# Optimization experiments

Hardware: AMD Instinct MI355X
Metric: run time of the kernel (lower is better)

## Reference

```python
import jax, jax.numpy as jnp
import numpy as np

N, E = 50000, 800000
IN, MID, OUT = 128, 256, 128
LN_EPS = 1e-5


def layer_norm(x, gamma, beta, eps=LN_EPS):
    mu = jnp.mean(x, axis=-1, keepdims=True)
    var = jnp.mean(jnp.square(x - mu), axis=-1, keepdims=True)
    return (x - mu) * jax.lax.rsqrt(var + eps) * gamma + beta


def gcn_conv(x, W, b, src, dst, norm, n):
    # x' = D^{-1/2}(A+I)D^{-1/2} X W + b  (self-loops already folded into src/dst/norm)
    h = x @ W                                  # [N, F_out]
    msg = h[src] * norm[:, None]               # [E+N, F_out] gather + scale
    out = jax.ops.segment_sum(msg, dst, num_segments=n)
    return out + b


def setup_inputs() -> dict:
    key = jax.random.key(0)
    ks = jax.random.split(key, 4)
    x = jax.random.normal(ks[0], (N, IN), dtype=jnp.float32)
    edge_index = jax.random.randint(ks[1], (2, E), 0, N, dtype=jnp.int32)
    W1 = jax.random.normal(ks[2], (IN, MID), dtype=jnp.float32) * (1.0 / np.sqrt(IN))
    b1 = jnp.zeros((MID,), jnp.float32)
    g1 = jnp.ones((IN,), jnp.float32)
    be1 = jnp.zeros((IN,), jnp.float32)
    W4 = jax.random.normal(ks[3], (MID, OUT), dtype=jnp.float32) * (1.0 / np.sqrt(MID))
    b4 = jnp.zeros((OUT,), jnp.float32)
    g4 = jnp.ones((MID,), jnp.float32)
    be4 = jnp.zeros((MID,), jnp.float32)
    return {"x": x, "W1": W1, "b1": b1, "g1": g1, "be1": be1,
            "W4": W4, "b4": b4, "g4": g4, "be4": be4,
            "edge_index": edge_index}


def reference(x, W1, b1, g1, be1, W4, b4, g4, be4, edge_index):
    n = x.shape[0]
    loop = jnp.arange(n, dtype=edge_index.dtype)
    src = jnp.concatenate([edge_index[0], loop])   # [E+N]
    dst = jnp.concatenate([edge_index[1], loop])   # [E+N]
    deg = jax.ops.segment_sum(jnp.ones_like(src, x.dtype), dst, num_segments=n)
    dinv = jax.lax.rsqrt(deg)                      # deg >= 1 thanks to self-loops
    norm = dinv[src] * dinv[dst]                   # [E+N]

    h = gcn_conv(layer_norm(x, g1, be1), W1, b1, src, dst, norm, n)
    h = jax.nn.gelu(h, approximate=False)          # torch F.gelu default = exact erf
    h = gcn_conv(layer_norm(h, g4, be4), W4, b4, src, dst, norm, n)
    return h
```

## Files before the change

### kernel.cpp

```cpp
#include <hip/hip_runtime.h>
#include <math.h>

#define N_NODES 50000
#define E_EDGES 800000

typedef __attribute__((ext_vector_type(4))) float f32x4;
typedef __attribute__((ext_vector_type(8))) short s16x8;

#define T1_OFF    0UL
#define AGG1_OFF  12800000UL
#define T2B_OFF   38400000UL
#define WB1H_OFF  64000000UL
#define WB1L_OFF  64100096UL
#define WB4H_OFF  64200192UL
#define WB4L_OFF  64300288UL
#define DINV_OFF  64400384UL
#define HIST8_OFF 64600384UL
#define RP8_OFF   66200384UL
#define POSREL_OFF 67800448UL
#define CSRS_OFF  71000448UL
#define BSUM_OFF  74200448UL

__device__ __forceinline__ float lo16f(unsigned u) { return __uint_as_float(u << 16); }
__device__ __forceinline__ float hi16f(unsigned u) { return __uint_as_float(u & 0xffff0000u); }
__device__ __forceinline__ unsigned pack2bf(float a, float b) {
  unsigned ua = __float_as_uint(a); ua += 0x7fffu + ((ua >> 16) & 1u);
  unsigned ub = __float_as_uint(b); ub += 0x7fffu + ((ub >> 16) & 1u);
  return (ua >> 16) | (ub & 0xffff0000u);
}
__device__ __forceinline__ float gelu_f(float x) {
  return 0.5f * x * (1.f + erff(x * 0.70710678118654752f));
}

__global__ __launch_bounds__(256) void zero_hist8(int4* __restrict__ h) {
  int i = blockIdx.x * 256 + threadIdx.x;
  if (i < 100000) h[i] = make_int4(0, 0, 0, 0);
}

__global__ __launch_bounds__(256) void edge_pos(const int* __restrict__ dst,
                                                int* __restrict__ hist8,
                                                int* __restrict__ posrel) {
  int e = blockIdx.x * 256 + threadIdx.x;
  int d = dst[e];
  int seg = blockIdx.x & 7;
  int r = atomicAdd(&hist8[d * 8 + seg], 1);
  __builtin_nontemporal_store(r, posrel + e);
}

__global__ __launch_bounds__(1024) void scan_partial(const int* __restrict__ hist,
                                                     int* __restrict__ rp,
                                                     int* __restrict__ bsum, int n) {
  __shared__ int wsum[16];
  int tid = threadIdx.x, lane = tid & 63, wv = tid >> 6;
  int i = blockIdx.x * 1024 + tid;
  int v = (i < n) ? hist[i] : 0;
  int sc = v;
  #pragma unroll
  for (int m = 1; m < 64; m <<= 1) { int o = __shfl_up(sc, m); if (lane >= m) sc += o; }
  if (lane == 63) wsum[wv] = sc;
  __syncthreads();
  if (wv == 0) {
    int w = (lane < 16) ? wsum[lane] : 0;
    int swc = w;
    #pragma unroll
    for (int m = 1; m < 16; m <<= 1) { int o = __shfl_up(swc, m); if (lane >= m) swc += o; }
    if (lane < 16) wsum[lane] = swc - w;
    if (lane == 15) bsum[blockIdx.x] = swc;
  }
  __syncthreads();
  if (i < n) rp[i] = (sc - v) + wsum[wv];
}

__global__ __launch_bounds__(64) void scan_bsums(int* __restrict__ bsum, int nb) {
  int lane = threadIdx.x;
  int carry = 0;
  for (int base = 0; base < nb; base += 64) {
    int i = base + lane;
    int v = (i < nb) ? bsum[i] : 0;
    int sc = v;
    #pragma unroll
    for (int m = 1; m < 64; m <<= 1) { int o = __shfl_up(sc, m); if (lane >= m) sc += o; }
    if (i < nb) bsum[i] = carry + sc - v;
    carry += __shfl(sc, 63);
  }
  if (lane == 0) bsum[nb] = carry;
}

__global__ __launch_bounds__(1024) void scan_add(int* __restrict__ rp,
                                                 const int* __restrict__ bsum, int n) {
  int i = blockIdx.x * 1024 + threadIdx.x;
  if (i < n) rp[i] += bsum[blockIdx.x];
  if (i == 0) rp[n] = bsum[gridDim.x];
}

__global__ __launch_bounds__(256) void dinv_kernel(const int* __restrict__ rp8,
                                                   float* __restrict__ dinv, int n) {
  int i = blockIdx.x * 256 + threadIdx.x;
  if (i < n) {
    int deg = rp8[i * 8 + 8] - rp8[i * 8];
    dinv[i] = rsqrtf((float)(deg + 1));
  }
}

__global__ __launch_bounds__(256) void fill2(const int* __restrict__ src,
                                             const int* __restrict__ dst,
                                             const int* __restrict__ rp8,
                                             const int* __restrict__ posrel,
                                             int* __restrict__ csr_src) {
  int e = blockIdx.x * 256 + threadIdx.x;
  int s = src[e], d = dst[e];
  int seg = blockIdx.x & 7;
  int pos = rp8[d * 8 + seg] + posrel[e];
  __builtin_nontemporal_store(s, csr_src + pos);
}

__global__ __launch_bounds__(256) void convW_split(const float* __restrict__ W,
                                                   unsigned* __restrict__ Wh,
                                                   unsigned* __restrict__ Wl, int K, int N) {
  int tid = blockIdx.x * 256 + threadIdx.x;
  if (tid >= (K * N) / 8) return;
  int c15 = tid & 15;
  int kg  = (tid >> 4) & 3;
  int KS  = K >> 5;
  int ks  = (tid >> 6) % KS;
  int nt  = (tid >> 6) / KS;
  int col = nt * 16 + c15;
  int k0  = ks * 32 + kg * 8;
  float w[8];
  #pragma unroll
  for (int j = 0; j < 8; ++j) w[j] = W[(size_t)(k0 + j) * N + col];
  uint4 h, l;
  h.x = pack2bf(w[0], w[1]); l.x = pack2bf(w[0] - lo16f(h.x), w[1] - hi16f(h.x));
  h.y = pack2bf(w[2], w[3]); l.y = pack2bf(w[2] - lo16f(h.y), w[3] - hi16f(h.y));
  h.z = pack2bf(w[4], w[5]); l.z = pack2bf(w[4] - lo16f(h.z), w[5] - hi16f(h.z));
  h.w = pack2bf(w[6], w[7]); l.w = pack2bf(w[6] - lo16f(h.w), w[7] - hi16f(h.w));
  *reinterpret_cast<uint4*>(Wh + (size_t)tid * 4) = h;
  *reinterpret_cast<uint4*>(Wl + (size_t)tid * 4) = l;
}

__global__ __launch_bounds__(256) void ln1_kernel(const float* __restrict__ x,
                                                  const float* __restrict__ g,
                                                  const float* __restrict__ be,
                                                  unsigned* __restrict__ T) {
  int lane = threadIdx.x & 63, wv = threadIdx.x >> 6;
  int row = blockIdx.x * 4 + wv;
  float2 v = *reinterpret_cast<const float2*>(x + (size_t)row * 128 + lane * 2);
  float s = v.x + v.y, sq = v.x * v.x + v.y * v.y;
  #pragma unroll
  for (int m = 1; m < 64; m <<= 1) { s += __shfl_xor(s, m); sq += __shfl_xor(sq, m); }
  float mu = s * (1.f / 128.f);
  float var = sq * (1.f / 128.f) - mu * mu;
  float rs = rsqrtf(var + 1e-5f);
  float2 gg = *reinterpret_cast<const float2*>(g + lane * 2);
  float2 bb = *reinterpret_cast<const float2*>(be + lane * 2);
  T[(size_t)row * 64 + lane] =
      pack2bf((v.x - mu) * rs * gg.x + bb.x, (v.y - mu) * rs * gg.y + bb.y);
}

template <int MODE>
__global__ __launch_bounds__(256) void agg128(const unsigned* __restrict__ T,
                                              const int* __restrict__ rp8,
                                              const int* __restrict__ csr_src,
                                              const float* __restrict__ dinv,
                                              const float* __restrict__ b,
                                              float* __restrict__ out) {
  int lane = threadIdx.x & 63, wv = threadIdx.x >> 6;
  int node = blockIdx.x * 4 + wv;
  float di = dinv[node], sn = di * di;
  unsigned us = T[(size_t)node * 64 + lane];
  float a0 = lo16f(us) * sn, a1 = hi16f(us) * sn;
  int e = rp8[node * 8], e1 = rp8[node * 8 + 8];
  for (; e + 3 < e1; e += 4) {
    int4 c = *reinterpret_cast<const int4*>(csr_src + e);
    unsigned u0 = T[(size_t)c.x * 64 + lane];
    unsigned u1 = T[(size_t)c.y * 64 + lane];
    unsigned u2 = T[(size_t)c.z * 64 + lane];
    unsigned u3 = T[(size_t)c.w * 64 + lane];
    float n0 = dinv[c.x] * di, n1 = dinv[c.y] * di;
    float n2 = dinv[c.z] * di, n3 = dinv[c.w] * di;
    a0 += lo16f(u0) * n0; a1 += hi16f(u0) * n0;
    a0 += lo16f(u1) * n1; a1 += hi16f(u1) * n1;
    a0 += lo16f(u2) * n2; a1 += hi16f(u2) * n2;
    a0 += lo16f(u3) * n3; a1 += hi16f(u3) * n3;
  }
  for (; e < e1; ++e) {
    int s = csr_src[e];
    unsigned u = T[(size_t)s * 64 + lane];
    float nr = dinv[s] * di;
    a0 += lo16f(u) * nr; a1 += hi16f(u) * nr;
  }
  if (MODE == 0) {
    *reinterpret_cast<float2*>(out + (size_t)node * 128 + lane * 2) = make_float2(a0, a1);
  } else {
    float2 bb = *reinterpret_cast<const float2*>(b + lane * 2);
    *reinterpret_cast<float2*>(out + (size_t)node * 128 + lane * 2) =
        make_float2(a0 + bb.x, a1 + bb.y);
  }
}

__global__ __launch_bounds__(256) void gemm1_fused(const float* __restrict__ A,
                                                   const unsigned* __restrict__ Wh,
                                                   const unsigned* __restrict__ Wl,
                                                   const float* __restrict__ b,
                                                   const float* __restrict__ g,
                                                   const float* __restrict__ be,
                                                   unsigned* __restrict__ T2b, int n) {
  __shared__ float st[32 * 260];
  int t = threadIdx.x, lane = t & 63, w = t >> 6;
  int rtile = (w >> 1) * 16;
  int c0 = (w & 1) * 128;
  int arow = blockIdx.x * 32 + rtile + (lane & 15);
  if (arow >= n) arow = n - 1;
  const float* aptr = A + (size_t)arow * 128 + (lane >> 4) * 8;
  f32x4 acc[8];
  #pragma unroll
  for (int nf = 0; nf < 8; ++nf) acc[nf] = (f32x4)(0.f);
  #pragma unroll
  for (int ks = 0; ks < 4; ++ks) {
    float4 v0 = *reinterpret_cast<const float4*>(aptr + ks * 32);
    float4 v1 = *reinterpret_cast<const float4*>(aptr + ks * 32 + 4);
    uint4 h, l;
    h.x = pack2bf(v0.x, v0.y); l.x = pack2bf(v0.x - lo16f(h.x), v0.y - hi16f(h.x));
    h.y = pack2bf(v0.z, v0.w); l.y = pack2bf(v0.z - lo16f(h.y), v0.w - hi16f(h.y));
    h.z = pack2bf(v1.x, v1.y); l.z = pack2bf(v1.x - lo16f(h.z), v1.y - hi16f(h.z));
    h.w = pack2bf(v1.z, v1.w); l.w = pack2bf(v1.z - lo16f(h.w), v1.w - hi16f(h.w));
    s16x8 ah = *reinterpret_cast<s16x8*>(&h);
    s16x8 al = *reinterpret_cast<s16x8*>(&l);
    #pragma unroll
    for (int nf = 0; nf < 8; ++nf) {
      int nt = (c0 >> 4) + nf;
      size_t bo = (size_t)(((nt * 4 + ks) * 4 + (lane >> 4)) * 16 + (lane & 15)) * 4;
      s16x8 bh = *reinterpret_cast<const s16x8*>(Wh + bo);
      s16x8 bl = *reinterpret_cast<const s16x8*>(Wl + bo);
      acc[nf] = __builtin_amdgcn_mfma_f32_16x16x32_bf16(ah, bh, acc[nf], 0, 0, 0);
      acc[nf] = __builtin_amdgcn_mfma_f32_16x16x32_bf16(al, bh, acc[nf], 0, 0, 0);
      acc[nf] = __builtin_amdgcn_mfma_f32_16x16x32_bf16(ah, bl, acc[nf], 0, 0, 0);
    }
  }
  #pragma unroll
  for (int nf = 0; nf < 8; ++nf) {
    int col = c0 + nf * 16 + (lane & 15);
    float bb = b[col];
    #pragma unroll
    for (int r = 0; r < 4; ++r) {
      int row = rtile + (lane >> 4) * 4 + r;
      st[row * 260 + col] = gelu_f(acc[nf][r] + bb);
    }
  }
  __syncthreads();
  float4 gg = *reinterpret_cast<const float4*>(g + lane * 4);
  float4 bb2 = *reinterpret_cast<const float4*>(be + lane * 4);
  #pragma unroll
  for (int rr = 0; rr < 8; ++rr) {
    int row = w * 8 + rr;
    float4 v = *reinterpret_cast<const float4*>(&st[row * 260 + lane * 4]);
    float s = v.x + v.y + v.z + v.w;
    float sq = v.x * v.x + v.y * v.y + v.z * v.z + v.w * v.w;
    #pragma unroll
    for (int m = 1; m < 64; m <<= 1) { s += __shfl_xor(s, m); sq += __shfl_xor(sq, m); }
    float mu = s * (1.f / 256.f);
    float var = sq * (1.f / 256.f) - mu * mu;
    float rs = rsqrtf(var + 1e-5f);
    int gr = blockIdx.x * 32 + row;
    if (gr < n) {
      uint2 p;
      p.x = pack2bf((v.x - mu) * rs * gg.x + bb2.x, (v.y - mu) * rs * gg.y + bb2.y);
      p.y = pack2bf((v.z - mu) * rs * gg.z + bb2.z, (v.w - mu) * rs * gg.w + bb2.w);
      *reinterpret_cast<uint2*>(T2b + (size_t)gr * 128 + lane * 2) = p;
    }
  }
}

__global__ __launch_bounds__(256) void gemm2_mfma(const unsigned* __restrict__ Ab,
                                                  const unsigned* __restrict__ Wh,
                                                  const unsigned* __restrict__ Wl,
                                                  unsigned* __restrict__ T2, int n) {
  __shared__ float st[32 * 132];
  int t = threadIdx.x, lane = t & 63, w = t >> 6;
  int rtile = (w >> 1) * 16;
  int c0 = (w & 1) * 64;
  int arow = blockIdx.x * 32 + rtile + (lane & 15);
  if (arow >= n) arow = n - 1;
  const unsigned* aptr = Ab + (size_t)arow * 128 + (lane >> 4) * 4;
  f32x4 acc[4];
  #pragma unroll
  for (int nf = 0; nf < 4; ++nf) acc[nf] = (f32x4)(0.f);
  #pragma unroll
  for (int ks = 0; ks < 8; ++ks) {
    s16x8 af = *reinterpret_cast<const s16x8*>(aptr + ks * 16);
    #pragma unroll
    for (int nf = 0; nf < 4; ++nf) {
      int nt = (c0 >> 4) + nf;
      size_t bo = (size_t)(((nt * 8 + ks) * 4 + (lane >> 4)) * 16 + (lane & 15)) * 4;
      s16x8 bh = *reinterpret_cast<const s16x8*>(Wh + bo);
      s16x8 bl = *reinterpret_cast<const s16x8*>(Wl + bo);
      acc[nf] = __builtin_amdgcn_mfma_f32_16x16x32_bf16(af, bh, acc[nf], 0, 0, 0);
      acc[nf] = __builtin_amdgcn_mfma_f32_16x16x32_bf16(af, bl, acc[nf], 0, 0, 0);
    }
  }
  #pragma unroll
  for (int nf = 0; nf < 4; ++nf) {
    int col = c0 + nf * 16 + (lane & 15);
    #pragma unroll
    for (int r = 0; r < 4; ++r) {
      int row = rtile + (lane >> 4) * 4 + r;
      st[row * 132 + col] = acc[nf][r];
    }
  }
  __syncthreads();
  #pragma unroll
  for (int rr = 0; rr < 8; ++rr) {
    int row = w * 8 + rr;
    int gr = blockIdx.x * 32 + row;
    if (gr < n) {
      float2 v = *reinterpret_cast<const float2*>(&st[row * 132 + lane * 2]);
      T2[(size_t)gr * 64 + lane] = pack2bf(v.x, v.y);
    }
  }
}

extern "C" void kernel_launch(void* const* d_in, const int* in_sizes, int n_in,
                              void* d_out, int out_size, void* d_ws, size_t ws_size,
                              hipStream_t stream) {
  (void)in_sizes; (void)n_in; (void)out_size; (void)ws_size;
  const float* x   = (const float*)d_in[0];
  const float* W1  = (const float*)d_in[1];
  const float* b1  = (const float*)d_in[2];
  const float* g1  = (const float*)d_in[3];
  const float* be1 = (const float*)d_in[4];
  const float* W4  = (const float*)d_in[5];
  const float* b4  = (const float*)d_in[6];
  const float* g4  = (const float*)d_in[7];
  const float* be4 = (const float*)d_in[8];
  const int*   ei  = (const int*)d_in[9];
  const int* src = ei;
  const int* dst = ei + E_EDGES;

  char* ws = (char*)d_ws;
  unsigned* T1    = (unsigned*)(ws + T1_OFF);
  unsigned* T2    = (unsigned*)(ws + T1_OFF);
  float*    AGG1  = (float*)(ws + AGG1_OFF);
  unsigned* T2b   = (unsigned*)(ws + T2B_OFF);
  unsigned* Wb1h  = (unsigned*)(ws + WB1H_OFF);
  unsigned* Wb1l  = (unsigned*)(ws + WB1L_OFF);
  unsigned* Wb4h  = (unsigned*)(ws + WB4H_OFF);
  unsigned* Wb4l  = (unsigned*)(ws + WB4L_OFF);
  float* dinv     = (float*)(ws + DINV_OFF);
  int*   hist8    = (int*)(ws + HIST8_OFF);
  int*   rp8      = (int*)(ws + RP8_OFF);
  int*   posrel   = (int*)(ws + POSREL_OFF);
  int*   csr_src  = (int*)(ws + CSRS_OFF);
  int*   bsum     = (int*)(ws + BSUM_OFF);
  float* outp     = (float*)d_out;

  const int NSEG = N_NODES * 8;
  int nblkE  = E_EDGES / 256;
  int nbScan = (NSEG + 1023) / 1024;
  int nblkG  = (N_NODES + 31) / 32;

  hipLaunchKernelGGL(zero_hist8, dim3(391), dim3(256), 0, stream, (int4*)hist8);
  hipLaunchKernelGGL(edge_pos, dim3(nblkE), dim3(256), 0, stream, dst, hist8, posrel);
  hipLaunchKernelGGL(scan_partial, dim3(nbScan), dim3(1024), 0, stream, hist8, rp8, bsum, NSEG);
  hipLaunchKernelGGL(scan_bsums, dim3(1), dim3(64), 0, stream, bsum, nbScan);
  hipLaunchKernelGGL(scan_add, dim3(nbScan), dim3(1024), 0, stream, rp8, bsum, NSEG);
  hipLaunchKernelGGL(dinv_kernel, dim3((N_NODES + 255) / 256), dim3(256), 0, stream,
                     rp8, dinv, N_NODES);
  hipLaunchKernelGGL(fill2, dim3(nblkE), dim3(256), 0, stream, src, dst, rp8, posrel, csr_src);
  hipLaunchKernelGGL(convW_split, dim3(16), dim3(256), 0, stream, W1, Wb1h, Wb1l, 128, 256);
  hipLaunchKernelGGL(convW_split, dim3(16), dim3(256), 0, stream, W4, Wb4h, Wb4l, 256, 128);

  hipLaunchKernelGGL(ln1_kernel, dim3(N_NODES / 4), dim3(256), 0, stream, x, g1, be1, T1);
  hipLaunchKernelGGL(agg128<0>, dim3(N_NODES / 4), dim3(256), 0, stream,
                     T1, rp8, csr_src, dinv, (const float*)nullptr, AGG1);
  hipLaunchKernelGGL(gemm1_fused, dim3(nblkG), dim3(256), 0, stream,
                     AGG1, Wb1h, Wb1l, b1, g4, be4, T2b, N_NODES);

  hipLaunchKernelGGL(gemm2_mfma, dim3(nblkG), dim3(256), 0, stream, T2b, Wb4h, Wb4l, T2, N_NODES);
  hipLaunchKernelGGL(agg128<2>, dim3(N_NODES / 4), dim3(256), 0, stream,
                     T2, rp8, csr_src, dinv, b4, outp);
}
```

Baseline: 234.0 us.

## Emit split-bf16 aggregates and retile GEMM warps to reuse weight fragments

The first aggregation now writes its fp32 result as pre-split bf16 hi/lo arrays, so gemm1 no longer converts fp32 A on the fly. Both GEMMs are retiled so each warp covers 32 rows and a narrower column band, which halves the per-warp weight-fragment loads relative to the MFMA count. The degree computation now reads the per-node histogram directly instead of the scanned row pointers. Storage for the intermediate stays the same size, but gemm1's A is now read from two arrays and the split rounding happens in the aggregation epilogue.

```diff
diff --git a/kernel.cpp b/kernel.cpp
--- a/kernel.cpp
+++ b/kernel.cpp
@@ -8,7 +8,8 @@
 typedef __attribute__((ext_vector_type(8))) short s16x8;
 
 #define T1_OFF    0UL
-#define AGG1_OFF  12800000UL
+#define A1H_OFF   12800000UL
+#define A1L_OFF   25600000UL
 #define T2B_OFF   38400000UL
 #define WB1H_OFF  64000000UL
 #define WB1L_OFF  64100096UL
@@ -93,11 +94,13 @@
   if (i == 0) rp[n] = bsum[gridDim.x];
 }
 
-__global__ __launch_bounds__(256) void dinv_kernel(const int* __restrict__ rp8,
+__global__ __launch_bounds__(256) void dinv_kernel(const int* __restrict__ hist8,
                                                    float* __restrict__ dinv, int n) {
   int i = blockIdx.x * 256 + threadIdx.x;
   if (i < n) {
-    int deg = rp8[i * 8 + 8] - rp8[i * 8];
+    int4 a = *reinterpret_cast<const int4*>(hist8 + i * 8);
+    int4 b = *reinterpret_cast<const int4*>(hist8 + i * 8 + 4);
+    int deg = a.x + a.y + a.z + a.w + b.x + b.y + b.z + b.w;
     dinv[i] = rsqrtf((float)(deg + 1));
   }
 }
@@ -163,7 +166,9 @@
                                               const int* __restrict__ csr_src,
                                               const float* __restrict__ dinv,
                                               const float* __restrict__ b,
-                                              float* __restrict__ out) {
+                                              float* __restrict__ out,
+                                              unsigned* __restrict__ outh,
+                                              unsigned* __restrict__ outl) {
   int lane = threadIdx.x & 63, wv = threadIdx.x >> 6;
   int node = blockIdx.x * 4 + wv;
   float di = dinv[node], sn = di * di;
@@ -190,7 +195,10 @@
     a0 += lo16f(u) * nr; a1 += hi16f(u) * nr;
   }
   if (MODE == 0) {
-    *reinterpret_cast<float2*>(out + (size_t)node * 128 + lane * 2) = make_float2(a0, a1);
+    unsigned h = pack2bf(a0, a1);
+    float r0 = a0 - lo16f(h), r1 = a1 - hi16f(h);
+    outh[(size_t)node * 64 + lane] = h;
+    outl[(size_t)node * 64 + lane] = pack2bf(r0, r1);
   } else {
     float2 bb = *reinterpret_cast<const float2*>(b + lane * 2);
     *reinterpret_cast<float2*>(out + (size_t)node * 128 + lane * 2) =
@@ -198,7 +206,8 @@
   }
 }
 
-__global__ __launch_bounds__(256) void gemm1_fused(const float* __restrict__ A,
+__global__ __launch_bounds__(256) void gemm1_fused(const unsigned* __restrict__ Ah,
+                                                   const unsigned* __restrict__ Al,
                                                    const unsigned* __restrict__ Wh,
                                                    const unsigned* __restrict__ Wl,
                                                    const float* __restrict__ b,
@@ -207,46 +216,56 @@
                                                    unsigned* __restrict__ T2b, int n) {
   __shared__ float st[32 * 260];
   int t = threadIdx.x, lane = t & 63, w = t >> 6;
-  int rtile = (w >> 1) * 16;
-  int c0 = (w & 1) * 128;
-  int arow = blockIdx.x * 32 + rtile + (lane & 15);
-  if (arow >= n) arow = n - 1;
-  const float* aptr = A + (size_t)arow * 128 + (lane >> 4) * 8;
-  f32x4 acc[8];
-  #pragma unroll
-  for (int nf = 0; nf < 8; ++nf) acc[nf] = (f32x4)(0.f);
+  int kg = lane >> 4, c15 = lane & 15;
+  int c0 = w * 64;
+  int row0 = blockIdx.x * 32 + c15;
+  int r0 = min(row0, n - 1);
+  int r1 = min(row0 + 16, n - 1);
+  const unsigned* ah0 = Ah + (size_t)r0 * 64 + kg * 4;
+  const unsigned* al0 = Al + (size_t)r0 * 64 + kg * 4;
+  const unsigned* ah1 = Ah + (size_t)r1 * 64 + kg * 4;
+  const unsigned* al1 = Al + (size_t)r1 * 64 + kg * 4;
+  f32x4 acc[2][4];
+  #pragma unroll
+  for (int rt = 0; rt < 2; ++rt)
+    #pragma unroll
+    for (int nf = 0; nf < 4; ++nf) acc[rt][nf] = (f32x4)(0.f);
   #pragma unroll
   for (int ks = 0; ks < 4; ++ks) {
-    float4 v0 = *reinterpret_cast<const float4*>(aptr + ks * 32);
-    float4 v1 = *reinterpret_cast<const float4*>(aptr + ks * 32 + 4);
-    uint4 h, l;
-    h.x = pack2bf(v0.x, v0.y); l.x = pack2bf(v0.x - lo16f(h.x), v0.y - hi16f(h.x));
-    h.y = pack2bf(v0.z, v0.w); l.y = pack2bf(v0.z - lo16f(h.y), v0.w - hi16f(h.y));
-    h.z = pack2bf(v1.x, v1.y); l.z = pack2bf(v1.x - lo16f(h.z), v1.y - hi16f(h.z));
-    h.w = pack2bf(v1.z, v1.w); l.w = pack2bf(v1.z - lo16f(h.w), v1.w - hi16f(h.w));
-    s16x8 ah = *reinterpret_cast<s16x8*>(&h);
-    s16x8 al = *reinterpret_cast<s16x8*>(&l);
-    #pragma unroll
-    for (int nf = 0; nf < 8; ++nf) {
+    s16x8 bh[4], bl[4];
+    #pragma unroll
+    for (int nf = 0; nf < 4; ++nf) {
       int nt = (c0 >> 4) + nf;
-      size_t bo = (size_t)(((nt * 4 + ks) * 4 + (lane >> 4)) * 16 + (lane & 15)) * 4;
-      s16x8 bh = *reinterpret_cast<const s16x8*>(Wh + bo);
-      s16x8 bl = *reinterpret_cast<const s16x8*>(Wl + bo);
-      acc[nf] = __builtin_amdgcn_mfma_f32_16x16x32_bf16(ah, bh, acc[nf], 0, 0, 0);
-      acc[nf] = __builtin_amdgcn_mfma_f32_16x16x32_bf16(al, bh, acc[nf], 0, 0, 0);
-      acc[nf] = __builtin_amdgcn_mfma_f32_16x16x32_bf16(ah, bl, acc[nf], 0, 0, 0);
-    }
-  }
-  #pragma unroll
-  for (int nf = 0; nf < 8; ++nf) {
-    int col = c0 + nf * 16 + (lane & 15);
-    float bb = b[col];
-    #pragma unroll
-    for (int r = 0; r < 4; ++r) {
-      int row = rtile + (lane >> 4) * 4 + r;
-      st[row * 260 + col] = gelu_f(acc[nf][r] + bb);
-    }
-  }
+      size_t bo = (size_t)(((nt * 4 + ks) * 4 + kg) * 16 + c15) * 4;
+      bh[nf] = *reinterpret_cast<const s16x8*>(Wh + bo);
+      bl[nf] = *reinterpret_cast<const s16x8*>(Wl + bo);
+    }
+    s16x8 a0h = *reinterpret_cast<const s16x8*>(ah0 + ks * 16);
+    s16x8 a0l = *reinterpret_cast<const s16x8*>(al0 + ks * 16);
+    s16x8 a1h = *reinterpret_cast<const s16x8*>(ah1 + ks * 16);
+    s16x8 a1l = *reinterpret_cast<const s16x8*>(al1 + ks * 16);
+    #pragma unroll
+    for (int nf = 0; nf < 4; ++nf) {
+      acc[0][nf] = __builtin_amdgcn_mfma_f32_16x16x32_bf16(a0h, bh[nf], acc[0][nf], 0, 0, 0);
+      acc[0][nf] = __builtin_amdgcn_mfma_f32_16x16x32_bf16(a0l, bh[nf], acc[0][nf], 0, 0, 0);
+      acc[0][nf] = __builtin_amdgcn_mfma_f32_16x16x32_bf16(a0h, bl[nf], acc[0][nf], 0, 0, 0);
+      acc[1][nf] = __builtin_amdgcn_mfma_f32_16x16x32_bf16(a1h, bh[nf], acc[1][nf], 0, 0, 0);
+      acc[1][nf] = __builtin_amdgcn_mfma_f32_16x16x32_bf16(a1l, bh[nf], acc[1][nf], 0, 0, 0);
+      acc[1][nf] = __builtin_amdgcn_mfma_f32_16x16x32_bf16(a1h, bl[nf], acc[1][nf], 0, 0, 0);
+    }
+  }
+  #pragma unroll
+  for (int rt = 0; rt < 2; ++rt)
+    #pragma unroll
+    for (int nf = 0; nf < 4; ++nf) {
+      int col = c0 + nf * 16 + c15;
+      float bb = b[col];
+      #pragma unroll
+      for (int r = 0; r < 4; ++r) {
+        int row = rt * 16 + kg * 4 + r;
+        st[row * 260 + col] = gelu_f(acc[rt][nf][r] + bb);
+      }
+    }
   __syncthreads();
   float4 gg = *reinterpret_cast<const float4*>(g + lane * 4);
   float4 bb2 = *reinterpret_cast<const float4*>(be + lane * 4);
@@ -277,36 +296,47 @@
                                                   unsigned* __restrict__ T2, int n) {
   __shared__ float st[32 * 132];
   int t = threadIdx.x, lane = t & 63, w = t >> 6;
-  int rtile = (w >> 1) * 16;
-  int c0 = (w & 1) * 64;
-  int arow = blockIdx.x * 32 + rtile + (lane & 15);
-  if (arow >= n) arow = n - 1;
-  const unsigned* aptr = Ab + (size_t)arow * 128 + (lane >> 4) * 4;
-  f32x4 acc[4];
-  #pragma unroll
-  for (int nf = 0; nf < 4; ++nf) acc[nf] = (f32x4)(0.f);
+  int kg = lane >> 4, c15 = lane & 15;
+  int c0 = w * 32;
+  int row0 = blockIdx.x * 32 + c15;
+  int r0 = min(row0, n - 1);
+  int r1 = min(row0 + 16, n - 1);
+  const unsigned* ap0 = Ab + (size_t)r0 * 128 + kg * 4;
+  const unsigned* ap1 = Ab + (size_t)r1 * 128 + kg * 4;
+  f32x4 acc[2][2];
+  #pragma unroll
+  for (int rt = 0; rt < 2; ++rt) { acc[rt][0] = (f32x4)(0.f); acc[rt][1] = (f32x4)(0.f); }
   #pragma unroll
   for (int ks = 0; ks < 8; ++ks) {
-    s16x8 af = *reinterpret_cast<const s16x8*>(aptr + ks * 16);
-    #pragma unroll
-    for (int nf = 0; nf < 4; ++nf) {
+    s16x8 bh[2], bl[2];
+    #pragma unroll
+    for (int nf = 0; nf < 2; ++nf) {
       int nt = (c0 >> 4) + nf;
-      size_t bo = (size_t)(((nt * 8 + ks) * 4 + (lane >> 4)) * 16 + (lane & 15)) * 4;
-      s16x8 bh = *reinterpret_cast<const s16x8*>(Wh + bo);
-      s16x8 bl = *reinterpret_cast<const s16x8*>(Wl + bo);
-      acc[nf] = __builtin_amdgcn_mfma_f32_16x16x32_bf16(af, bh, acc[nf], 0, 0, 0);
-      acc[nf] = __builtin_amdgcn_mfma_f32_16x16x32_bf16(af, bl, acc[nf], 0, 0, 0);
-    }
-  }
-  #pragma unroll
-  for (int nf = 0; nf < 4; ++nf) {
-    int col = c0 + nf * 16 + (lane & 15);
-    #pragma unroll
-    for (int r = 0; r < 4; ++r) {
-      int row = rtile + (lane >> 4) * 4 + r;
-      st[row * 132 + col] = acc[nf][r];
-    }
-  }
+      size_t bo = (size_t)(((nt * 8 + ks) * 4 + kg) * 16 + c15) * 4;
+      bh[nf] = *reinterpret_cast<const s16x8*>(Wh + bo);
+      bl[nf] = *reinterpret_cast<const s16x8*>(Wl + bo);
+    }
+    s16x8 a0 = *reinterpret_cast<const s16x8*>(ap0 + ks * 16);
+    s16x8 a1 = *reinterpret_cast<const s16x8*>(ap1 + ks * 16);
+    #pragma unroll
+    for (int nf = 0; nf < 2; ++nf) {
+      acc[0][nf] = __builtin_amdgcn_mfma_f32_16x16x32_bf16(a0, bh[nf], acc[0][nf], 0, 0, 0);
+      acc[0][nf] = __builtin_amdgcn_mfma_f32_16x16x32_bf16(a0, bl[nf], acc[0][nf], 0, 0, 0);
+      acc[1][nf] = __builtin_amdgcn_mfma_f32_16x16x32_bf16(a1, bh[nf], acc[1][nf], 0, 0, 0);
+      acc[1][nf] = __builtin_amdgcn_mfma_f32_16x16x32_bf16(a1, bl[nf], acc[1][nf], 0, 0, 0);
+    }
+  }
+  #pragma unroll
+  for (int rt = 0; rt < 2; ++rt)
+    #pragma unroll
+    for (int nf = 0; nf < 2; ++nf) {
+      int col = c0 + nf * 16 + c15;
+      #pragma unroll
+      for (int r = 0; r < 4; ++r) {
+        int row = rt * 16 + kg * 4 + r;
+        st[row * 132 + col] = acc[rt][nf][r];
+      }
+    }
   __syncthreads();
   #pragma unroll
   for (int rr = 0; rr < 8; ++rr) {
@@ -339,7 +369,8 @@
   char* ws = (char*)d_ws;
   unsigned* T1    = (unsigned*)(ws + T1_OFF);
   unsigned* T2    = (unsigned*)(ws + T1_OFF);
-  float*    AGG1  = (float*)(ws + AGG1_OFF);
+  unsigned* A1h   = (unsigned*)(ws + A1H_OFF);
+  unsigned* A1l   = (unsigned*)(ws + A1L_OFF);
   unsigned* T2b   = (unsigned*)(ws + T2B_OFF);
   unsigned* Wb1h  = (unsigned*)(ws + WB1H_OFF);
   unsigned* Wb1l  = (unsigned*)(ws + WB1L_OFF);
@@ -360,22 +391,24 @@
 
   hipLaunchKernelGGL(zero_hist8, dim3(391), dim3(256), 0, stream, (int4*)hist8);
   hipLaunchKernelGGL(edge_pos, dim3(nblkE), dim3(256), 0, stream, dst, hist8, posrel);
+  hipLaunchKernelGGL(dinv_kernel, dim3((N_NODES + 255) / 256), dim3(256), 0, stream,
+                     hist8, dinv, N_NODES);
   hipLaunchKernelGGL(scan_partial, dim3(nbScan), dim3(1024), 0, stream, hist8, rp8, bsum, NSEG);
   hipLaunchKernelGGL(scan_bsums, dim3(1), dim3(64), 0, stream, bsum, nbScan);
   hipLaunchKernelGGL(scan_add, dim3(nbScan), dim3(1024), 0, stream, rp8, bsum, NSEG);
-  hipLaunchKernelGGL(dinv_kernel, dim3((N_NODES + 255) / 256), dim3(256), 0, stream,
-                     rp8, dinv, N_NODES);
   hipLaunchKernelGGL(fill2, dim3(nblkE), dim3(256), 0, stream, src, dst, rp8, posrel, csr_src);
   hipLaunchKernelGGL(convW_split, dim3(16), dim3(256), 0, stream, W1, Wb1h, Wb1l, 128, 256);
   hipLaunchKernelGGL(convW_split, dim3(16), dim3(256), 0, stream, W4, Wb4h, Wb4l, 256, 128);
 
   hipLaunchKernelGGL(ln1_kernel, dim3(N_NODES / 4), dim3(256), 0, stream, x, g1, be1, T1);
   hipLaunchKernelGGL(agg128<0>, dim3(N_NODES / 4), dim3(256), 0, stream,
-                     T1, rp8, csr_src, dinv, (const float*)nullptr, AGG1);
+                     T1, rp8, csr_src, dinv, (const float*)nullptr,
+                     (float*)nullptr, A1h, A1l);
   hipLaunchKernelGGL(gemm1_fused, dim3(nblkG), dim3(256), 0, stream,
-                     AGG1, Wb1h, Wb1l, b1, g4, be4, T2b, N_NODES);
+                     A1h, A1l, Wb1h, Wb1l, b1, g4, be4, T2b, N_NODES);
 
   hipLaunchKernelGGL(gemm2_mfma, dim3(nblkG), dim3(256), 0, stream, T2b, Wb4h, Wb4l, T2, N_NODES);
   hipLaunchKernelGGL(agg128<2>, dim3(N_NODES / 4), dim3(256), 0, stream,
-                     T2, rp8, csr_src, dinv, b4, outp);
-}
+                     T2, rp8, csr_src, dinv, b4, outp,
+                     (unsigned*)nullptr, (unsigned*)nullptr);
+}
```

Measured after the change: 231.9 us. About the same (-0.9%).
